# Performance work log

Hardware: AMD Instinct MI355X
Metric: run time of the kernel (lower is better)

Reference implementation:

```python
import jax, jax.numpy as jnp
import numpy as np

C = 201        # n_classes + 1 (background)
K = 5          # prototypes per class
DIM = 768
B = 64
HP = 16        # patch grid side, n_patches = HP*HP
N_PATCH = HP * HP
GAMMA = 0.999
SK_ITERS = 3
EPS = 1e-12


def setup_inputs() -> dict:
    key = jax.random.key(0)
    k1, k2, k3, k4 = jax.random.split(key, 4)
    return dict(
        patch_tokens=jax.random.normal(k1, (B, N_PATCH, DIM), jnp.float32),
        prototypes=jax.random.normal(k2, (C, K, DIM), jnp.float32) * 0.02,  # trunc_normal(std=0.02) approx
        sa=jnp.full((C - 1, K), 0.5, jnp.float32),                          # sa_init=0.5
        scale=jnp.float32(4.0),                                             # scale_init=4.0
        labels=jax.random.randint(k3, (B,), 0, C - 1),                      # image-level labels in [0, 200)
        masks=jax.random.bernoulli(k4, 0.5, (B, HP, HP)),                   # fg_extractor output
    )


def _masked_sinkhorn(L, m, n_iters=SK_ITERS):
    """Sinkhorn-Knopp over a masked subset of rows.
    L: [N, K] logits, m: [N] bool row mask. Rows outside m stay zero.
    Equivalent to running SK on the gathered rows L[m] (softmax init,
    alternating column/row normalization)."""
    Q = jax.nn.softmax(L, axis=-1) * m[:, None]

    def body(Q, _):
        Q = Q / (Q.sum(axis=0, keepdims=True) + EPS)                         # column normalize
        Q = jnp.where(m[:, None], Q / (Q.sum(axis=1, keepdims=True) + EPS), 0.0)  # row normalize (masked rows)
        return Q, None

    Q, _ = jax.lax.scan(body, Q, None, length=n_iters)
    return Q


def reference(patch_tokens, prototypes, sa, scale, labels, masks):
    # --- cosine patch-prototype logits ---
    tok = patch_tokens / (jnp.linalg.norm(patch_tokens, axis=-1, keepdims=True) + EPS)
    pro = prototypes / (jnp.linalg.norm(prototypes, axis=-1, keepdims=True) + EPS)
    patch_prototype_logits = jnp.einsum('bnd,ckd->bnck', tok, pro)           # [B, N, C, K]

    # --- avg pooling over patches ---
    image_prototype_logits = patch_prototype_logits.mean(axis=1)             # [B, C, K]

    # --- 'sa' classification head ---
    sa_w = jax.nn.softmax(sa, axis=-1) * K                                   # [C-1, K]
    class_logits = (scale * image_prototype_logits[:, :-1, :] * sa_w).sum(-1)  # [B, C-1]

    # --- pseudo patch labels from fg masks ---
    pseudo_patch_labels = jnp.where(masks, labels[:, None, None], C - 1)     # [B, H, W] int
    pl_flat = pseudo_patch_labels.reshape(-1)                                # [B*N]

    # --- online clustering (operates on detached values in the original) ---
    tok_flat = jax.lax.stop_gradient(tok).reshape(-1, DIM)                   # [B*N, D]
    L_flat = jax.lax.stop_gradient(patch_prototype_logits).reshape(-1, C, K)  # [B*N, C, K]
    class_mask = pl_flat[None, :] == jnp.arange(C)[:, None]                  # [C, B*N]

    # vectorized per-class masked Sinkhorn-Knopp (replaces dynamic python loop over unique labels)
    Q_all = jax.vmap(_masked_sinkhorn, in_axes=(1, 0))(L_flat, class_mask)   # [C, B*N, K]

    # prototype candidates: P_c_new = L_c_assignment^T @ I_c (masked rows are zero)
    P_new_c = jnp.einsum('cnk,nd->ckd', Q_all, tok_flat)                     # [C, K, D]
    has_class = class_mask.any(axis=1)[:, None, None]
    new_prototypes = jnp.where(has_class,
                               GAMMA * prototypes + (1.0 - GAMMA) * P_new_c,
                               prototypes)

    # part assignment: argmax over K, gathered at each patch's own class
    idx_all = jnp.argmax(Q_all, axis=-1)                                     # [C, B*N]
    part_assignment_maps = idx_all[pl_flat, jnp.arange(pl_flat.shape[0])].reshape(B, N_PATCH)

    return (patch_prototype_logits, image_prototype_logits, class_logits,
            part_assignment_maps, new_prototypes, pseudo_patch_labels)
```

## Files before the change

kernel.cpp:

```cpp
#include <hip/hip_runtime.h>
#include <math.h>

#define NTOK 16384
#define NPRO 1005
#define DIMD 768
#define CKD  1005
#define CC   201
#define KKp  5
#define BGC  200
#define KEXP 2304
#define KA   1536
#define NPAD 1024

#define OUT_LOGITS   0
#define OUT_IMG      16465920
#define OUT_CLS      (OUT_IMG + 64320)
#define OUT_PART     (OUT_CLS + 12800)
#define OUT_NEWPROTO (OUT_PART + 16384)
#define OUT_PSEUDO   (OUT_NEWPROTO + 771840)

#define WOFF_PACC    0
#define WOFF_COUNTS  3087360
#define WOFF_FLAG    3088384
#define WS_ZERO_B    3088640
#define WOFF_A2      3088640ULL
#define WOFF_B2      53420288ULL
#define WOFF_INVTOK  58138880ULL
#define WOFF_PL      58204416ULL
#define WOFF_Q       58269952ULL
#define WOFF_COLSUM  58597632ULL
#define WOFF_OFFSETS 58601728ULL
#define WOFF_CURSORS 58602752ULL
#define WOFF_ORDER   58603776ULL

typedef __attribute__((ext_vector_type(8))) short short8;
typedef __attribute__((ext_vector_type(4))) float f32x4;
typedef __attribute__((ext_vector_type(4))) unsigned short usv4;

__device__ __forceinline__ unsigned short f2bf(float x) {
  unsigned int b = __float_as_uint(x);
  unsigned int r = (b + 0x7FFFu + ((b >> 16) & 1u)) >> 16;
  return (unsigned short)r;
}
__device__ __forceinline__ float bf2f(unsigned short u) {
  return __uint_as_float(((unsigned int)u) << 16);
}

__device__ __forceinline__ void async_copy16(const void* g, void* lds) {
  __builtin_amdgcn_global_load_lds(
      (const __attribute__((address_space(1))) unsigned int*)g,
      (__attribute__((address_space(3))) unsigned int*)lds, 16, 0, 0);
}

__global__ __launch_bounds__(256) void conv_tok_kernel(const float* __restrict__ tok,
                                                       unsigned short* __restrict__ A2,
                                                       float* __restrict__ inv_tok) {
  int wid = (blockIdx.x * 256 + threadIdx.x) >> 6;
  int lane = threadIdx.x & 63;
  if (wid >= NTOK) return;
  const float4* s4 = (const float4*)(tok + (size_t)wid * DIMD);
  float4 v[3];
  float s = 0.0f;
#pragma unroll
  for (int p = 0; p < 3; ++p) {
    v[p] = s4[p * 64 + lane];
    s += v[p].x * v[p].x + v[p].y * v[p].y + v[p].z * v[p].z + v[p].w * v[p].w;
  }
#pragma unroll
  for (int off = 32; off; off >>= 1) s += __shfl_xor(s, off, 64);
  float inv = 1.0f / (sqrtf(s) + 1e-12f);
  if (lane == 0) inv_tok[wid] = inv;
  unsigned short* rowp = A2 + (size_t)wid * KA;
#pragma unroll
  for (int p = 0; p < 3; ++p) {
    float x0 = v[p].x * inv, x1 = v[p].y * inv, x2 = v[p].z * inv, x3 = v[p].w * inv;
    usv4 hi, lo;
    hi.x = f2bf(x0); hi.y = f2bf(x1); hi.z = f2bf(x2); hi.w = f2bf(x3);
    lo.x = f2bf(x0 - bf2f(hi.x)); lo.y = f2bf(x1 - bf2f(hi.y));
    lo.z = f2bf(x2 - bf2f(hi.z)); lo.w = f2bf(x3 - bf2f(hi.w));
    int c = p * 256 + lane * 4;
    *(usv4*)(rowp + c) = hi;
    *(usv4*)(rowp + 768 + c) = lo;
  }
}

__global__ __launch_bounds__(256) void conv_pro_kernel(const float* __restrict__ pro,
                                                       unsigned short* __restrict__ B2) {
  int wid = (blockIdx.x * 256 + threadIdx.x) >> 6;
  int lane = threadIdx.x & 63;
  if (wid >= NPAD) return;
  unsigned short* rowp = B2 + (size_t)wid * KEXP;
  if (wid >= NPRO) {
    usv4 z = {0, 0, 0, 0};
#pragma unroll
    for (int p = 0; p < 3; ++p) {
      int c = p * 256 + lane * 4;
      *(usv4*)(rowp + c) = z; *(usv4*)(rowp + 768 + c) = z; *(usv4*)(rowp + 1536 + c) = z;
    }
    return;
  }
  const float4* s4 = (const float4*)(pro + (size_t)wid * DIMD);
  float4 v[3];
  float s = 0.0f;
#pragma unroll
  for (int p = 0; p < 3; ++p) {
    v[p] = s4[p * 64 + lane];
    s += v[p].x * v[p].x + v[p].y * v[p].y + v[p].z * v[p].z + v[p].w * v[p].w;
  }
#pragma unroll
  for (int off = 32; off; off >>= 1) s += __shfl_xor(s, off, 64);
  float inv = 1.0f / (sqrtf(s) + 1e-12f);
#pragma unroll
  for (int p = 0; p < 3; ++p) {
    float x0 = v[p].x * inv, x1 = v[p].y * inv, x2 = v[p].z * inv, x3 = v[p].w * inv;
    usv4 hi, lo;
    hi.x = f2bf(x0); hi.y = f2bf(x1); hi.z = f2bf(x2); hi.w = f2bf(x3);
    lo.x = f2bf(x0 - bf2f(hi.x)); lo.y = f2bf(x1 - bf2f(hi.y));
    lo.z = f2bf(x2 - bf2f(hi.z)); lo.w = f2bf(x3 - bf2f(hi.w));
    int c = p * 256 + lane * 4;
    *(usv4*)(rowp + c) = hi;
    *(usv4*)(rowp + 768 + c) = hi;
    *(usv4*)(rowp + 1536 + c) = lo;
  }
}

__global__ void maskprobe_kernel(const unsigned* __restrict__ masks, int* __restrict__ flag) {
  int i = blockIdx.x * 256 + threadIdx.x;
  if (i < 4096) {
    unsigned v = masks[i];
    if (v == 0x3F800000u)      atomicOr(flag, 1);
    else if (v > 1u)           atomicOr(flag, 2);
  }
}

__global__ __launch_bounds__(256, 2) void gemm_kernel(const unsigned short* __restrict__ A2,
                                                      const unsigned short* __restrict__ B2,
                                                      float* __restrict__ C,
                                                      float* __restrict__ img) {
  __shared__ unsigned short As[2][4096];
  __shared__ unsigned short Bs[2][4096];
  const int tid = threadIdx.x;
  const int lane = tid & 63, wave = tid >> 6;
  const int m0 = blockIdx.x * 128, n0 = blockIdx.y * 128;
  const int wr = wave >> 1, wc = wave & 1;

  f32x4 acc[4][4];
#pragma unroll
  for (int i = 0; i < 4; ++i)
#pragma unroll
    for (int j = 0; j < 4; ++j) acc[i][j] = (f32x4){0.f, 0.f, 0.f, 0.f};

  const int r4 = lane >> 2;
  const int kc = (lane & 3) * 8;

  auto STAGE = [&](int buf, int kt) {
    int kb = kt * 32;
    int acol = (kb < KA ? kb : kb - KA) + kc;
    int bcol = kb + kc;
#pragma unroll
    for (int j = 0; j < 2; ++j) {
      int seg = wave * 2 + j;
      async_copy16(A2 + (size_t)(m0 + seg * 16 + r4) * KA + acol, &As[buf][seg * 512]);
      async_copy16(B2 + (size_t)(n0 + seg * 16 + r4) * KEXP + bcol, &Bs[buf][seg * 512]);
    }
  };

  STAGE(0, 0);
  __syncthreads();

  const int rb = wr * 64 + (lane & 15);
  const int cb = wc * 64 + (lane & 15);
  const int hi8 = (lane >> 4) * 8;

  int cur = 0;
  for (int kt = 0; kt < 72; ++kt) {
    if (kt < 71) STAGE(cur ^ 1, kt + 1);
    short8 a[4], b[4];
#pragma unroll
    for (int f = 0; f < 4; ++f) {
      a[f] = *(const short8*)&As[cur][(rb + f * 16) * 32 + hi8];
      b[f] = *(const short8*)&Bs[cur][(cb + f * 16) * 32 + hi8];
    }
#pragma unroll
    for (int fm = 0; fm < 4; ++fm)
#pragma unroll
      for (int fn = 0; fn < 4; ++fn)
        acc[fm][fn] = __builtin_amdgcn_mfma_f32_16x16x32_bf16(a[fm], b[fn], acc[fm][fn], 0, 0, 0);
    __syncthreads();
    cur ^= 1;
  }

  const int bimg = m0 >> 8;
#pragma unroll
  for (int fn = 0; fn < 4; ++fn) {
    int col = n0 + wc * 64 + fn * 16 + (lane & 15);
    float s = 0.0f;
#pragma unroll
    for (int fm = 0; fm < 4; ++fm) {
      int row = m0 + wr * 64 + fm * 16 + (lane >> 4) * 4;
      f32x4 v = acc[fm][fn];
      if (col < NPRO) {
        C[(size_t)(row + 0) * CKD + col] = v.x;
        C[(size_t)(row + 1) * CKD + col] = v.y;
        C[(size_t)(row + 2) * CKD + col] = v.z;
        C[(size_t)(row + 3) * CKD + col] = v.w;
      }
      s += v.x + v.y + v.z + v.w;
    }
    s += __shfl_xor(s, 16, 64);
    s += __shfl_xor(s, 32, 64);
    if (lane < 16 && col < NPRO)
      atomicAdd(&img[bimg * CKD + col], s * (1.0f / 256.0f));
  }
}

__global__ __launch_bounds__(256) void cls_kernel(const float* __restrict__ img,
                                                  const float* __restrict__ sa,
                                                  const float* __restrict__ scale,
                                                  float* __restrict__ out_cls) {
  int gid = blockIdx.x * 256 + threadIdx.x;
  if (gid >= 64 * 200) return;
  int b = gid / 200, c = gid - b * 200;
  float s5[KKp];
  float mx = -1e30f;
#pragma unroll
  for (int k = 0; k < KKp; ++k) { s5[k] = sa[c * KKp + k]; mx = fmaxf(mx, s5[k]); }
  float den = 0.0f;
#pragma unroll
  for (int k = 0; k < KKp; ++k) { s5[k] = expf(s5[k] - mx); den += s5[k]; }
  float acc = 0.0f;
#pragma unroll
  for (int k = 0; k < KKp; ++k)
    acc += img[(size_t)b * CKD + c * KKp + k] * (s5[k] / den * 5.0f);
  out_cls[gid] = scale[0] * acc;
}

__global__ __launch_bounds__(256) void pseudo_kernel(const void* __restrict__ masks,
                                                     const int* __restrict__ labels,
                                                     const float* __restrict__ L,
                                                     const int* __restrict__ flag,
                                                     int* __restrict__ pl,
                                                     float* __restrict__ out_pseudo,
                                                     float* __restrict__ Q,
                                                     int* __restrict__ counts) {
  __shared__ int hist[CC];
  int t = threadIdx.x;
  if (t < CC) hist[t] = 0;
  __syncthreads();
  int n = blockIdx.x * 256 + t;
  int f = *flag;
  int m;
  if (f & 1)      m = ((const float*)masks)[n] != 0.0f;
  else if (f & 2) m = ((const unsigned char*)masks)[n] != 0;
  else            m = ((const int*)masks)[n] != 0;
  int lab = m ? labels[n >> 8] : BGC;
  pl[n] = lab;
  out_pseudo[n] = (float)lab;
  atomicAdd(&hist[lab], 1);
  const float* Lr = L + (size_t)n * CKD + lab * KKp;
  float q[KKp];
  float mx = -1e30f;
#pragma unroll
  for (int k = 0; k < KKp; ++k) { q[k] = Lr[k]; mx = fmaxf(mx, q[k]); }
  float den = 0.0f;
#pragma unroll
  for (int k = 0; k < KKp; ++k) { q[k] = expf(q[k] - mx); den += q[k]; }
  float inv = 1.0f / den;
#pragma unroll
  for (int k = 0; k < KKp; ++k) Q[(size_t)n * KKp + k] = q[k] * inv;
  __syncthreads();
  if (t < CC && hist[t] > 0) atomicAdd(&counts[t], hist[t]);
}

__global__ void prefix_kernel(const int* __restrict__ counts, int* __restrict__ offsets,
                              int* __restrict__ cursors) {
  __shared__ int sc[256];
  int t = threadIdx.x;
  int v = (t < CC) ? counts[t] : 0;
  sc[t] = v;
  __syncthreads();
  for (int off = 1; off < 256; off <<= 1) {
    int u = (t >= off) ? sc[t - off] : 0;
    __syncthreads();
    sc[t] += u;
    __syncthreads();
  }
  if (t < CC) { int excl = sc[t] - v; offsets[t] = excl; cursors[t] = excl; }
  if (t == CC - 1) offsets[CC] = sc[t];
}

__global__ __launch_bounds__(256) void scatter_kernel(const int* __restrict__ pl,
                                                      int* __restrict__ cursors,
                                                      int* __restrict__ order) {
  __shared__ int hist[CC], base[CC];
  int t = threadIdx.x;
  for (int c = t; c < CC; c += 256) hist[c] = 0;
  __syncthreads();
  int n = blockIdx.x * 256 + t;
  int c = pl[n];
  int rank = atomicAdd(&hist[c], 1);
  __syncthreads();
  for (int cc = t; cc < CC; cc += 256)
    if (hist[cc] > 0) base[cc] = atomicAdd(&cursors[cc], hist[cc]);
  __syncthreads();
  order[base[c] + rank] = n;
}

__global__ __launch_bounds__(256) void colsum_kernel(const float* __restrict__ Q,
                                                     const int* __restrict__ order,
                                                     const int* __restrict__ offsets,
                                                     float* __restrict__ colsum) {
  int c = blockIdx.x;
  int s0 = offsets[c], e0 = offsets[c + 1];
  float a[KKp] = {0, 0, 0, 0, 0};
  for (int i = s0 + threadIdx.x; i < e0; i += 256) {
    int n = order[i];
    const float* q = Q + (size_t)n * KKp;
#pragma unroll
    for (int k = 0; k < KKp; ++k) a[k] += q[k];
  }
#pragma unroll
  for (int off = 32; off; off >>= 1)
#pragma unroll
    for (int k = 0; k < KKp; ++k) a[k] += __shfl_xor(a[k], off, 64);
  __shared__ float wsum[4][KKp];
  int lane = threadIdx.x & 63, w = threadIdx.x >> 6;
  if (lane == 0) {
#pragma unroll
    for (int k = 0; k < KKp; ++k) wsum[w][k] = a[k];
  }
  __syncthreads();
  if (threadIdx.x == 0) {
#pragma unroll
    for (int k = 0; k < KKp; ++k)
      colsum[c * KKp + k] = wsum[0][k] + wsum[1][k] + wsum[2][k] + wsum[3][k];
  }
}

__global__ __launch_bounds__(256) void rowupd_kernel(float* __restrict__ Q,
                                                     const int* __restrict__ pl,
                                                     const float* __restrict__ colsum) {
  int n = blockIdx.x * 256 + threadIdx.x;
  if (n >= NTOK) return;
  int c = pl[n];
  float q[KKp];
  float r = 0.0f;
#pragma unroll
  for (int k = 0; k < KKp; ++k) {
    q[k] = Q[(size_t)n * KKp + k] / (colsum[c * KKp + k] + 1e-12f);
    r += q[k];
  }
  float rinv = 1.0f / (r + 1e-12f);
#pragma unroll
  for (int k = 0; k < KKp; ++k) Q[(size_t)n * KKp + k] = q[k] * rinv;
}

__global__ __launch_bounds__(256) void pnew_kernel(const int* __restrict__ order,
                                                   const int* __restrict__ pl,
                                                   const float* __restrict__ Q,
                                                   const float* __restrict__ tok,
                                                   const float* __restrict__ inv_tok,
                                                   float* __restrict__ P_acc) {
  __shared__ int idx[32], cls[32];
  int t = threadIdx.x;
  int p0 = blockIdx.x * 32;
  if (t < 32) {
    int n = order[p0 + t];
    idx[t] = n;
    cls[t] = pl[n];
  }
  __syncthreads();
  float acc[KKp][3];
#pragma unroll
  for (int k = 0; k < KKp; ++k)
#pragma unroll
    for (int s = 0; s < 3; ++s) acc[k][s] = 0.0f;
  int cur = cls[0];
  for (int i = 0; i < 32; ++i) {
    int c = cls[i];
    if (c != cur) {
#pragma unroll
      for (int k = 0; k < KKp; ++k)
#pragma unroll
        for (int s = 0; s < 3; ++s) {
          atomicAdd(&P_acc[((size_t)cur * KKp + k) * DIMD + s * 256 + t], acc[k][s]);
          acc[k][s] = 0.0f;
        }
      cur = c;
    }
    int n = idx[i];
    float it = inv_tok[n];
    float q[KKp];
#pragma unroll
    for (int k = 0; k < KKp; ++k) q[k] = Q[(size_t)n * KKp + k];
#pragma unroll
    for (int s = 0; s < 3; ++s) {
      float v = tok[(size_t)n * DIMD + s * 256 + t] * it;
#pragma unroll
      for (int k = 0; k < KKp; ++k) acc[k][s] = fmaf(q[k], v, acc[k][s]);
    }
  }
#pragma unroll
  for (int k = 0; k < KKp; ++k)
#pragma unroll
    for (int s = 0; s < 3; ++s)
      atomicAdd(&P_acc[((size_t)cur * KKp + k) * DIMD + s * 256 + t], acc[k][s]);
}

__global__ __launch_bounds__(256) void newproto_kernel(const float* __restrict__ proto,
                                                       const float* __restrict__ P_acc,
                                                       const int* __restrict__ counts,
                                                       float* __restrict__ outp) {
  int gid = blockIdx.x * 256 + threadIdx.x;
  if (gid >= CC * KKp * DIMD) return;
  int c = gid / (KKp * DIMD);
  float p = proto[gid];
  outp[gid] = (counts[c] > 0) ? (0.999f * p + 0.001f * P_acc[gid]) : p;
}

__global__ __launch_bounds__(256) void argmax_kernel(const float* __restrict__ Q,
                                                     float* __restrict__ out_part) {
  int n = blockIdx.x * 256 + threadIdx.x;
  if (n >= NTOK) return;
  float best = Q[(size_t)n * KKp];
  int bi = 0;
#pragma unroll
  for (int k = 1; k < KKp; ++k) {
    float v = Q[(size_t)n * KKp + k];
    if (v > best) { best = v; bi = k; }
  }
  out_part[n] = (float)bi;
}

extern "C" void kernel_launch(void* const* d_in, const int* in_sizes, int n_in,
                              void* d_out, int out_size, void* d_ws, size_t ws_size,
                              hipStream_t stream) {
  const float* patch_tokens = (const float*)d_in[0];
  const float* prototypes   = (const float*)d_in[1];
  const float* sa           = (const float*)d_in[2];
  const float* scale        = (const float*)d_in[3];
  const int*   labels       = (const int*)d_in[4];
  const void*  masks        = (const void*)d_in[5];

  float* out = (float*)d_out;
  float* out_logits  = out + OUT_LOGITS;
  float* out_img     = out + OUT_IMG;
  float* out_cls     = out + OUT_CLS;
  float* out_part    = out + OUT_PART;
  float* out_newp    = out + OUT_NEWPROTO;
  float* out_pseudo  = out + OUT_PSEUDO;

  char* w = (char*)d_ws;
  float*          P_acc   = (float*)(w + WOFF_PACC);
  int*            counts  = (int*)(w + WOFF_COUNTS);
  int*            flag    = (int*)(w + WOFF_FLAG);
  unsigned short* A2      = (unsigned short*)(w + WOFF_A2);
  unsigned short* B2      = (unsigned short*)(w + WOFF_B2);
  float*          inv_tok = (float*)(w + WOFF_INVTOK);
  int*            pl      = (int*)(w + WOFF_PL);
  float*          Q       = (float*)(w + WOFF_Q);
  float*          colsum  = (float*)(w + WOFF_COLSUM);
  int*            offsets = (int*)(w + WOFF_OFFSETS);
  int*            cursors = (int*)(w + WOFF_CURSORS);
  int*            order   = (int*)(w + WOFF_ORDER);

  hipMemsetAsync(d_ws, 0, WS_ZERO_B, stream);
  hipMemsetAsync(out_img, 0, (size_t)64 * CKD * sizeof(float), stream);

  maskprobe_kernel<<<16, 256, 0, stream>>>((const unsigned*)masks, flag);
  conv_tok_kernel<<<4096, 256, 0, stream>>>(patch_tokens, A2, inv_tok);
  conv_pro_kernel<<<256, 256, 0, stream>>>(prototypes, B2);

  gemm_kernel<<<dim3(128, 8), 256, 0, stream>>>(A2, B2, out_logits, out_img);

  cls_kernel<<<50, 256, 0, stream>>>(out_img, sa, scale, out_cls);

  pseudo_kernel<<<64, 256, 0, stream>>>(masks, labels, out_logits, flag,
                                        pl, out_pseudo, Q, counts);
  prefix_kernel<<<1, 256, 0, stream>>>(counts, offsets, cursors);
  scatter_kernel<<<64, 256, 0, stream>>>(pl, cursors, order);

  for (int it = 0; it < 3; ++it) {
    colsum_kernel<<<CC, 256, 0, stream>>>(Q, order, offsets, colsum);
    rowupd_kernel<<<64, 256, 0, stream>>>(Q, pl, colsum);
  }

  pnew_kernel<<<512, 256, 0, stream>>>(order, pl, Q, patch_tokens, inv_tok, P_acc);
  newproto_kernel<<<3015, 256, 0, stream>>>(prototypes, P_acc, counts, out_newp);
  argmax_kernel<<<64, 256, 0, stream>>>(Q, out_part);
}
```

Baseline: 335.0 us.

## Fuse small pre/post kernels: single-block prep, merged conv, per-class fused Sinkhorn

Merges the token and prototype conversion kernels into one launch. Replaces the mask probe, pseudo-label, prefix and scatter kernels with a single 1024-thread block that builds the labels, histogram, offsets and order. The three-iteration colsum/rowupd launch pairs, the softmax init and the argmax now run in one per-class block kernel, and the small workspace memset is dropped. This cuts about a dozen tiny launches, but the single-block prep and the per-class Sinkhorn blocks serialize work, and the background class holds roughly half the tokens in one block.

Measured after the change: 379.7 us. +13.3%, slower.

```diff
diff --git a/kernel.cpp b/kernel.cpp
--- a/kernel.cpp
+++ b/kernel.cpp
@@ -19,19 +19,14 @@
 #define OUT_NEWPROTO (OUT_PART + 16384)
 #define OUT_PSEUDO   (OUT_NEWPROTO + 771840)
 
-#define WOFF_PACC    0
-#define WOFF_COUNTS  3087360
-#define WOFF_FLAG    3088384
-#define WS_ZERO_B    3088640
-#define WOFF_A2      3088640ULL
-#define WOFF_B2      53420288ULL
-#define WOFF_INVTOK  58138880ULL
-#define WOFF_PL      58204416ULL
-#define WOFF_Q       58269952ULL
-#define WOFF_COLSUM  58597632ULL
-#define WOFF_OFFSETS 58601728ULL
-#define WOFF_CURSORS 58602752ULL
-#define WOFF_ORDER   58603776ULL
+#define WOFF_PACC    0ULL
+#define WOFF_A2      3087360ULL
+#define WOFF_B2      53419008ULL
+#define WOFF_INVTOK  58137600ULL
+#define WOFF_PL      58203136ULL
+#define WOFF_Q       58268672ULL
+#define WOFF_OFFSETS 58596352ULL
+#define WOFF_ORDER   58597376ULL
 
 typedef __attribute__((ext_vector_type(8))) short short8;
 typedef __attribute__((ext_vector_type(4))) float f32x4;
@@ -52,84 +47,150 @@
       (__attribute__((address_space(3))) unsigned int*)lds, 16, 0, 0);
 }
 
-__global__ __launch_bounds__(256) void conv_tok_kernel(const float* __restrict__ tok,
-                                                       unsigned short* __restrict__ A2,
-                                                       float* __restrict__ inv_tok) {
+__global__ __launch_bounds__(256) void conv_kernel(const float* __restrict__ tok,
+                                                   const float* __restrict__ pro,
+                                                   unsigned short* __restrict__ A2,
+                                                   unsigned short* __restrict__ B2,
+                                                   float* __restrict__ inv_tok) {
   int wid = (blockIdx.x * 256 + threadIdx.x) >> 6;
   int lane = threadIdx.x & 63;
-  if (wid >= NTOK) return;
-  const float4* s4 = (const float4*)(tok + (size_t)wid * DIMD);
-  float4 v[3];
-  float s = 0.0f;
-#pragma unroll
-  for (int p = 0; p < 3; ++p) {
-    v[p] = s4[p * 64 + lane];
-    s += v[p].x * v[p].x + v[p].y * v[p].y + v[p].z * v[p].z + v[p].w * v[p].w;
-  }
-#pragma unroll
-  for (int off = 32; off; off >>= 1) s += __shfl_xor(s, off, 64);
-  float inv = 1.0f / (sqrtf(s) + 1e-12f);
-  if (lane == 0) inv_tok[wid] = inv;
-  unsigned short* rowp = A2 + (size_t)wid * KA;
-#pragma unroll
-  for (int p = 0; p < 3; ++p) {
-    float x0 = v[p].x * inv, x1 = v[p].y * inv, x2 = v[p].z * inv, x3 = v[p].w * inv;
-    usv4 hi, lo;
-    hi.x = f2bf(x0); hi.y = f2bf(x1); hi.z = f2bf(x2); hi.w = f2bf(x3);
-    lo.x = f2bf(x0 - bf2f(hi.x)); lo.y = f2bf(x1 - bf2f(hi.y));
-    lo.z = f2bf(x2 - bf2f(hi.z)); lo.w = f2bf(x3 - bf2f(hi.w));
-    int c = p * 256 + lane * 4;
-    *(usv4*)(rowp + c) = hi;
-    *(usv4*)(rowp + 768 + c) = lo;
-  }
-}
-
-__global__ __launch_bounds__(256) void conv_pro_kernel(const float* __restrict__ pro,
-                                                       unsigned short* __restrict__ B2) {
-  int wid = (blockIdx.x * 256 + threadIdx.x) >> 6;
-  int lane = threadIdx.x & 63;
-  if (wid >= NPAD) return;
-  unsigned short* rowp = B2 + (size_t)wid * KEXP;
-  if (wid >= NPRO) {
-    usv4 z = {0, 0, 0, 0};
+  if (wid >= NTOK + NPAD) return;
+
+  if (wid < NTOK) {
+    const float4* s4 = (const float4*)(tok + (size_t)wid * DIMD);
+    float4 v[3];
+    float s = 0.0f;
 #pragma unroll
     for (int p = 0; p < 3; ++p) {
+      v[p] = s4[p * 64 + lane];
+      s += v[p].x * v[p].x + v[p].y * v[p].y + v[p].z * v[p].z + v[p].w * v[p].w;
+    }
+#pragma unroll
+    for (int off = 32; off; off >>= 1) s += __shfl_xor(s, off, 64);
+    float inv = 1.0f / (sqrtf(s) + 1e-12f);
+    if (lane == 0) inv_tok[wid] = inv;
+    unsigned short* rowp = A2 + (size_t)wid * KA;
+#pragma unroll
+    for (int p = 0; p < 3; ++p) {
+      float x0 = v[p].x * inv, x1 = v[p].y * inv, x2 = v[p].z * inv, x3 = v[p].w * inv;
+      usv4 hi, lo;
+      hi.x = f2bf(x0); hi.y = f2bf(x1); hi.z = f2bf(x2); hi.w = f2bf(x3);
+      lo.x = f2bf(x0 - bf2f(hi.x)); lo.y = f2bf(x1 - bf2f(hi.y));
+      lo.z = f2bf(x2 - bf2f(hi.z)); lo.w = f2bf(x3 - bf2f(hi.w));
       int c = p * 256 + lane * 4;
-      *(usv4*)(rowp + c) = z; *(usv4*)(rowp + 768 + c) = z; *(usv4*)(rowp + 1536 + c) = z;
-    }
-    return;
-  }
-  const float4* s4 = (const float4*)(pro + (size_t)wid * DIMD);
-  float4 v[3];
-  float s = 0.0f;
-#pragma unroll
-  for (int p = 0; p < 3; ++p) {
-    v[p] = s4[p * 64 + lane];
-    s += v[p].x * v[p].x + v[p].y * v[p].y + v[p].z * v[p].z + v[p].w * v[p].w;
-  }
-#pragma unroll
-  for (int off = 32; off; off >>= 1) s += __shfl_xor(s, off, 64);
-  float inv = 1.0f / (sqrtf(s) + 1e-12f);
-#pragma unroll
-  for (int p = 0; p < 3; ++p) {
-    float x0 = v[p].x * inv, x1 = v[p].y * inv, x2 = v[p].z * inv, x3 = v[p].w * inv;
-    usv4 hi, lo;
-    hi.x = f2bf(x0); hi.y = f2bf(x1); hi.z = f2bf(x2); hi.w = f2bf(x3);
-    lo.x = f2bf(x0 - bf2f(hi.x)); lo.y = f2bf(x1 - bf2f(hi.y));
-    lo.z = f2bf(x2 - bf2f(hi.z)); lo.w = f2bf(x3 - bf2f(hi.w));
-    int c = p * 256 + lane * 4;
-    *(usv4*)(rowp + c) = hi;
-    *(usv4*)(rowp + 768 + c) = hi;
-    *(usv4*)(rowp + 1536 + c) = lo;
-  }
-}
-
-__global__ void maskprobe_kernel(const unsigned* __restrict__ masks, int* __restrict__ flag) {
-  int i = blockIdx.x * 256 + threadIdx.x;
-  if (i < 4096) {
-    unsigned v = masks[i];
-    if (v == 0x3F800000u)      atomicOr(flag, 1);
-    else if (v > 1u)           atomicOr(flag, 2);
+      *(usv4*)(rowp + c) = hi;
+      *(usv4*)(rowp + 768 + c) = lo;
+    }
+  } else {
+    int pw = wid - NTOK;
+    unsigned short* rowp = B2 + (size_t)pw * KEXP;
+    if (pw >= NPRO) {
+      usv4 z = {0, 0, 0, 0};
+#pragma unroll
+      for (int p = 0; p < 3; ++p) {
+        int c = p * 256 + lane * 4;
+        *(usv4*)(rowp + c) = z; *(usv4*)(rowp + 768 + c) = z; *(usv4*)(rowp + 1536 + c) = z;
+      }
+      return;
+    }
+    const float4* s4 = (const float4*)(pro + (size_t)pw * DIMD);
+    float4 v[3];
+    float s = 0.0f;
+#pragma unroll
+    for (int p = 0; p < 3; ++p) {
+      v[p] = s4[p * 64 + lane];
+      s += v[p].x * v[p].x + v[p].y * v[p].y + v[p].z * v[p].z + v[p].w * v[p].w;
+    }
+#pragma unroll
+    for (int off = 32; off; off >>= 1) s += __shfl_xor(s, off, 64);
+    float inv = 1.0f / (sqrtf(s) + 1e-12f);
+#pragma unroll
+    for (int p = 0; p < 3; ++p) {
+      float x0 = v[p].x * inv, x1 = v[p].y * inv, x2 = v[p].z * inv, x3 = v[p].w * inv;
+      usv4 hi, lo;
+      hi.x = f2bf(x0); hi.y = f2bf(x1); hi.z = f2bf(x2); hi.w = f2bf(x3);
+      lo.x = f2bf(x0 - bf2f(hi.x)); lo.y = f2bf(x1 - bf2f(hi.y));
+      lo.z = f2bf(x2 - bf2f(hi.z)); lo.w = f2bf(x3 - bf2f(hi.w));
+      int c = p * 256 + lane * 4;
+      *(usv4*)(rowp + c) = hi;
+      *(usv4*)(rowp + 768 + c) = hi;
+      *(usv4*)(rowp + 1536 + c) = lo;
+    }
+  }
+}
+
+__global__ __launch_bounds__(1024) void prep_kernel(const void* __restrict__ masks,
+                                                    const int* __restrict__ labels,
+                                                    int* __restrict__ pl,
+                                                    float* __restrict__ out_pseudo,
+                                                    int* __restrict__ offsets,
+                                                    int* __restrict__ order) {
+  __shared__ int hist[256];
+  __shared__ int cur[256];
+  __shared__ int flagS;
+  int t = threadIdx.x;
+  int lane = t & 63;
+  if (t < 256) hist[t] = 0;
+  if (t == 0) flagS = 0;
+  __syncthreads();
+
+  const unsigned* mu = (const unsigned*)masks;
+  unsigned pr = 0;
+  for (int i = t; i < 4096; i += 1024) {
+    unsigned v = mu[i];
+    if (v == 0x3F800000u)      pr |= 1;
+    else if (v > 1u)           pr |= 2;
+  }
+  if (pr) atomicOr(&flagS, (int)pr);
+  __syncthreads();
+  int f = flagS;
+
+  int lab[16];
+#pragma unroll
+  for (int r = 0; r < 16; ++r) {
+    int n = r * 1024 + t;
+    int m;
+    if (f & 1)      m = ((const float*)masks)[n] != 0.0f;
+    else if (f & 2) m = ((const unsigned char*)masks)[n] != 0;
+    else            m = ((const int*)masks)[n] != 0;
+    int l = m ? labels[n >> 8] : BGC;
+    lab[r] = l;
+    pl[n] = l;
+    out_pseudo[n] = (float)l;
+    atomicAdd(&hist[l], 1);
+  }
+  __syncthreads();
+
+  int own = (t < 256) ? hist[t] : 0;
+  for (int off = 1; off < 256; off <<= 1) {
+    int u = (t >= off && t < 256) ? hist[t - off] : 0;
+    __syncthreads();
+    if (t < 256) hist[t] += u;
+    __syncthreads();
+  }
+  if (t < 256) {
+    int excl = hist[t] - own;
+    cur[t] = excl;
+    if (t <= CC) offsets[t] = (t < CC) ? excl : hist[CC - 1];
+  }
+  if (t == CC - 1) offsets[CC] = hist[CC - 1];
+  __syncthreads();
+
+#pragma unroll
+  for (int r = 0; r < 16; ++r) {
+    int n = r * 1024 + t;
+    int l = lab[r];
+    unsigned long long mk = __ballot(l == BGC);
+    if (l == BGC) {
+      int rank = __popcll(mk & ((1ull << lane) - 1));
+      int leader = (int)(__ffsll((long long)mk) - 1);
+      int base = 0;
+      if (lane == leader) base = atomicAdd(&cur[BGC], (int)__popcll(mk));
+      base = __shfl(base, leader, 64);
+      order[base + rank] = n;
+    } else {
+      order[atomicAdd(&cur[l], 1)] = n;
+    }
   }
 }
 
@@ -177,9 +238,9 @@
     if (kt < 71) STAGE(cur ^ 1, kt + 1);
     short8 a[4], b[4];
 #pragma unroll
-    for (int f = 0; f < 4; ++f) {
-      a[f] = *(const short8*)&As[cur][(rb + f * 16) * 32 + hi8];
-      b[f] = *(const short8*)&Bs[cur][(cb + f * 16) * 32 + hi8];
+    for (int ff = 0; ff < 4; ++ff) {
+      a[ff] = *(const short8*)&As[cur][(rb + ff * 16) * 32 + hi8];
+      b[ff] = *(const short8*)&Bs[cur][(cb + ff * 16) * 32 + hi8];
     }
 #pragma unroll
     for (int fm = 0; fm < 4; ++fm)
@@ -235,124 +296,85 @@
   out_cls[gid] = scale[0] * acc;
 }
 
-__global__ __launch_bounds__(256) void pseudo_kernel(const void* __restrict__ masks,
-                                                     const int* __restrict__ labels,
-                                                     const float* __restrict__ L,
-                                                     const int* __restrict__ flag,
-                                                     int* __restrict__ pl,
-                                                     float* __restrict__ out_pseudo,
-                                                     float* __restrict__ Q,
-                                                     int* __restrict__ counts) {
-  __shared__ int hist[CC];
-  int t = threadIdx.x;
-  if (t < CC) hist[t] = 0;
-  __syncthreads();
-  int n = blockIdx.x * 256 + t;
-  int f = *flag;
-  int m;
-  if (f & 1)      m = ((const float*)masks)[n] != 0.0f;
-  else if (f & 2) m = ((const unsigned char*)masks)[n] != 0;
-  else            m = ((const int*)masks)[n] != 0;
-  int lab = m ? labels[n >> 8] : BGC;
-  pl[n] = lab;
-  out_pseudo[n] = (float)lab;
-  atomicAdd(&hist[lab], 1);
-  const float* Lr = L + (size_t)n * CKD + lab * KKp;
-  float q[KKp];
-  float mx = -1e30f;
-#pragma unroll
-  for (int k = 0; k < KKp; ++k) { q[k] = Lr[k]; mx = fmaxf(mx, q[k]); }
-  float den = 0.0f;
-#pragma unroll
-  for (int k = 0; k < KKp; ++k) { q[k] = expf(q[k] - mx); den += q[k]; }
-  float inv = 1.0f / den;
-#pragma unroll
-  for (int k = 0; k < KKp; ++k) Q[(size_t)n * KKp + k] = q[k] * inv;
-  __syncthreads();
-  if (t < CC && hist[t] > 0) atomicAdd(&counts[t], hist[t]);
-}
-
-__global__ void prefix_kernel(const int* __restrict__ counts, int* __restrict__ offsets,
-                              int* __restrict__ cursors) {
-  __shared__ int sc[256];
-  int t = threadIdx.x;
-  int v = (t < CC) ? counts[t] : 0;
-  sc[t] = v;
-  __syncthreads();
-  for (int off = 1; off < 256; off <<= 1) {
-    int u = (t >= off) ? sc[t - off] : 0;
-    __syncthreads();
-    sc[t] += u;
-    __syncthreads();
-  }
-  if (t < CC) { int excl = sc[t] - v; offsets[t] = excl; cursors[t] = excl; }
-  if (t == CC - 1) offsets[CC] = sc[t];
-}
-
-__global__ __launch_bounds__(256) void scatter_kernel(const int* __restrict__ pl,
-                                                      int* __restrict__ cursors,
-                                                      int* __restrict__ order) {
-  __shared__ int hist[CC], base[CC];
-  int t = threadIdx.x;
-  for (int c = t; c < CC; c += 256) hist[c] = 0;
-  __syncthreads();
-  int n = blockIdx.x * 256 + t;
-  int c = pl[n];
-  int rank = atomicAdd(&hist[c], 1);
-  __syncthreads();
-  for (int cc = t; cc < CC; cc += 256)
-    if (hist[cc] > 0) base[cc] = atomicAdd(&cursors[cc], hist[cc]);
-  __syncthreads();
-  order[base[c] + rank] = n;
-}
-
-__global__ __launch_bounds__(256) void colsum_kernel(const float* __restrict__ Q,
-                                                     const int* __restrict__ order,
-                                                     const int* __restrict__ offsets,
-                                                     float* __restrict__ colsum) {
+__global__ __launch_bounds__(256) void qsink_kernel(const float* __restrict__ L,
+                                                    const int* __restrict__ order,
+                                                    const int* __restrict__ offsets,
+                                                    float* __restrict__ Q,
+                                                    float* __restrict__ out_part) {
   int c = blockIdx.x;
   int s0 = offsets[c], e0 = offsets[c + 1];
-  float a[KKp] = {0, 0, 0, 0, 0};
-  for (int i = s0 + threadIdx.x; i < e0; i += 256) {
+  if (s0 >= e0) return;
+  int t = threadIdx.x;
+  int lane = t & 63, w = t >> 6;
+  __shared__ float cs[KKp];
+  __shared__ float wsum[4][KKp];
+
+  for (int i = s0 + t; i < e0; i += 256) {
     int n = order[i];
-    const float* q = Q + (size_t)n * KKp;
-#pragma unroll
-    for (int k = 0; k < KKp; ++k) a[k] += q[k];
-  }
-#pragma unroll
-  for (int off = 32; off; off >>= 1)
-#pragma unroll
-    for (int k = 0; k < KKp; ++k) a[k] += __shfl_xor(a[k], off, 64);
-  __shared__ float wsum[4][KKp];
-  int lane = threadIdx.x & 63, w = threadIdx.x >> 6;
-  if (lane == 0) {
-#pragma unroll
-    for (int k = 0; k < KKp; ++k) wsum[w][k] = a[k];
-  }
-  __syncthreads();
-  if (threadIdx.x == 0) {
-#pragma unroll
-    for (int k = 0; k < KKp; ++k)
-      colsum[c * KKp + k] = wsum[0][k] + wsum[1][k] + wsum[2][k] + wsum[3][k];
-  }
-}
-
-__global__ __launch_bounds__(256) void rowupd_kernel(float* __restrict__ Q,
-                                                     const int* __restrict__ pl,
-                                                     const float* __restrict__ colsum) {
-  int n = blockIdx.x * 256 + threadIdx.x;
-  if (n >= NTOK) return;
-  int c = pl[n];
-  float q[KKp];
-  float r = 0.0f;
-#pragma unroll
-  for (int k = 0; k < KKp; ++k) {
-    q[k] = Q[(size_t)n * KKp + k] / (colsum[c * KKp + k] + 1e-12f);
-    r += q[k];
-  }
-  float rinv = 1.0f / (r + 1e-12f);
-#pragma unroll
-  for (int k = 0; k < KKp; ++k) Q[(size_t)n * KKp + k] = q[k] * rinv;
+    const float* Lr = L + (size_t)n * CKD + c * KKp;
+    float q[KKp];
+    float mx = -1e30f;
+#pragma unroll
+    for (int k = 0; k < KKp; ++k) { q[k] = Lr[k]; mx = fmaxf(mx, q[k]); }
+    float den = 0.0f;
+#pragma unroll
+    for (int k = 0; k < KKp; ++k) { q[k] = expf(q[k] - mx); den += q[k]; }
+    float inv = 1.0f / den;
+#pragma unroll
+    for (int k = 0; k < KKp; ++k) Q[(size_t)n * KKp + k] = q[k] * inv;
+  }
+  __syncthreads();
+
+  for (int it = 0; it < 3; ++it) {
+    float a[KKp] = {0, 0, 0, 0, 0};
+    for (int i = s0 + t; i < e0; i += 256) {
+      int n = order[i];
+      const float* q = Q + (size_t)n * KKp;
+#pragma unroll
+      for (int k = 0; k < KKp; ++k) a[k] += q[k];
+    }
+#pragma unroll
+    for (int off = 32; off; off >>= 1)
+#pragma unroll
+      for (int k = 0; k < KKp; ++k) a[k] += __shfl_xor(a[k], off, 64);
+    if (lane == 0) {
+#pragma unroll
+      for (int k = 0; k < KKp; ++k) wsum[w][k] = a[k];
+    }
+    __syncthreads();
+    if (t == 0) {
+#pragma unroll
+      for (int k = 0; k < KKp; ++k)
+        cs[k] = wsum[0][k] + wsum[1][k] + wsum[2][k] + wsum[3][k];
+    }
+    __syncthreads();
+
+    for (int i = s0 + t; i < e0; i += 256) {
+      int n = order[i];
+      float q[KKp];
+      float r = 0.0f;
+#pragma unroll
+      for (int k = 0; k < KKp; ++k) {
+        q[k] = Q[(size_t)n * KKp + k] / (cs[k] + 1e-12f);
+        r += q[k];
+      }
+      float rinv = 1.0f / (r + 1e-12f);
+#pragma unroll
+      for (int k = 0; k < KKp; ++k) {
+        q[k] *= rinv;
+        Q[(size_t)n * KKp + k] = q[k];
+      }
+      if (it == 2) {
+        float best = q[0];
+        int bi = 0;
+#pragma unroll
+        for (int k = 1; k < KKp; ++k)
+          if (q[k] > best) { best = q[k]; bi = k; }
+        out_part[n] = (float)bi;
+      }
+    }
+    __syncthreads();
+  }
 }
 
 __global__ __launch_bounds__(256) void pnew_kernel(const int* __restrict__ order,
@@ -409,27 +431,14 @@
 
 __global__ __launch_bounds__(256) void newproto_kernel(const float* __restrict__ proto,
                                                        const float* __restrict__ P_acc,
-                                                       const int* __restrict__ counts,
+                                                       const int* __restrict__ offsets,
                                                        float* __restrict__ outp) {
   int gid = blockIdx.x * 256 + threadIdx.x;
   if (gid >= CC * KKp * DIMD) return;
   int c = gid / (KKp * DIMD);
   float p = proto[gid];
-  outp[gid] = (counts[c] > 0) ? (0.999f * p + 0.001f * P_acc[gid]) : p;
-}
-
-__global__ __launch_bounds__(256) void argmax_kernel(const float* __restrict__ Q,
-                                                     float* __restrict__ out_part) {
-  int n = blockIdx.x * 256 + threadIdx.x;
-  if (n >= NTOK) return;
-  float best = Q[(size_t)n * KKp];
-  int bi = 0;
-#pragma unroll
-  for (int k = 1; k < KKp; ++k) {
-    float v = Q[(size_t)n * KKp + k];
-    if (v > best) { best = v; bi = k; }
-  }
-  out_part[n] = (float)bi;
+  bool has = offsets[c + 1] > offsets[c];
+  outp[gid] = has ? (0.999f * p + 0.001f * P_acc[gid]) : p;
 }
 
 extern "C" void kernel_launch(void* const* d_in, const int* in_sizes, int n_in,
@@ -452,40 +461,25 @@
 
   char* w = (char*)d_ws;
   float*          P_acc   = (float*)(w + WOFF_PACC);
-  int*            counts  = (int*)(w + WOFF_COUNTS);
-  int*            flag    = (int*)(w + WOFF_FLAG);
   unsigned short* A2      = (unsigned short*)(w + WOFF_A2);
   unsigned short* B2      = (unsigned short*)(w + WOFF_B2);
   float*          inv_tok = (float*)(w + WOFF_INVTOK);
   int*            pl      = (int*)(w + WOFF_PL);
   float*          Q       = (float*)(w + WOFF_Q);
-  float*          colsum  = (float*)(w + WOFF_COLSUM);
   int*            offsets = (int*)(w + WOFF_OFFSETS);
-  int*            cursors = (int*)(w + WOFF_CURSORS);
   int*            order   = (int*)(w + WOFF_ORDER);
 
-  hipMemsetAsync(d_ws, 0, WS_ZERO_B, stream);
+  hipMemsetAsync(P_acc, 0, 3087360, stream);
   hipMemsetAsync(out_img, 0, (size_t)64 * CKD * sizeof(float), stream);
 
-  maskprobe_kernel<<<16, 256, 0, stream>>>((const unsigned*)masks, flag);
-  conv_tok_kernel<<<4096, 256, 0, stream>>>(patch_tokens, A2, inv_tok);
-  conv_pro_kernel<<<256, 256, 0, stream>>>(prototypes, B2);
+  prep_kernel<<<1, 1024, 0, stream>>>(masks, labels, pl, out_pseudo, offsets, order);
+  conv_kernel<<<4352, 256, 0, stream>>>(patch_tokens, prototypes, A2, B2, inv_tok);
 
   gemm_kernel<<<dim3(128, 8), 256, 0, stream>>>(A2, B2, out_logits, out_img);
 
   cls_kernel<<<50, 256, 0, stream>>>(out_img, sa, scale, out_cls);
-
-  pseudo_kernel<<<64, 256, 0, stream>>>(masks, labels, out_logits, flag,
-                                        pl, out_pseudo, Q, counts);
-  prefix_kernel<<<1, 256, 0, stream>>>(counts, offsets, cursors);
-  scatter_kernel<<<64, 256, 0, stream>>>(pl, cursors, order);
-
-  for (int it = 0; it < 3; ++it) {
-    colsum_kernel<<<CC, 256, 0, stream>>>(Q, order, offsets, colsum);
-    rowupd_kernel<<<64, 256, 0, stream>>>(Q, pl, colsum);
-  }
+  qsink_kernel<<<CC, 256, 0, stream>>>(out_logits, order, offsets, Q, out_part);
 
   pnew_kernel<<<512, 256, 0, stream>>>(order, pl, Q, patch_tokens, inv_tok, P_acc);
-  newproto_kernel<<<3015, 256, 0, stream>>>(prototypes, P_acc, counts, out_newp);
-  argmax_kernel<<<64, 256, 0, stream>>>(Q, out_part);
-}
+  newproto_kernel<<<3015, 256, 0, stream>>>(prototypes, P_acc, offsets, out_newp);
+}
```
